# Optimization experiments

Measured on AMD Instinct MI355X. Metric: run time of the kernel, lower is better.

The kernel has to match this reference:

```python
import jax, jax.numpy as jnp
import numpy as np

BS, TGT, SRC = 16, 100, 100
M, N, H = 512, 512, 256  # query_size, key_size, hidden (min//2)


def setup_inputs() -> dict:
    key = jax.random.key(0)
    ks = jax.random.split(key, 7)
    s1 = 1.0 / np.sqrt(M + N)  # torch Linear init scale for layer 1 (fan_in = 1024)
    s2 = 1.0 / np.sqrt(H)
    return {
        "query": jax.random.normal(ks[0], (BS, TGT, M), jnp.float32),
        "keys": jax.random.normal(ks[1], (BS, SRC, N), jnp.float32),
        # W1 (H, M+N) split into key-part and query-part (concat order is (keys, query))
        "Wk": jax.random.uniform(ks[2], (N, H), jnp.float32, -s1, s1),
        "Wq": jax.random.uniform(ks[3], (M, H), jnp.float32, -s1, s1),
        "b1": jax.random.uniform(ks[4], (H,), jnp.float32, -s1, s1),
        "W2": jax.random.uniform(ks[5], (H, 1), jnp.float32, -s2, s2),
        "b2": jax.random.uniform(ks[6], (1,), jnp.float32, -s2, s2),
    }


def reference(query, keys, Wk, Wq, b1, W2, b2):
    # Equivalent to concat([keys_bcast, query_bcast], -1) @ W1 + b1:
    # apply the split weight to each side, then broadcast-add over the grid.
    hk = jnp.einsum("bsn,nh->bsh", keys, Wk)   # (bs, src, H)
    hq = jnp.einsum("btm,mh->bth", query, Wq)  # (bs, tgt, H)
    h = jnp.tanh(hk[:, :, None, :] + hq[:, None, :, :] + b1)  # (bs, src, tgt, H)
    score = jnp.tanh(jnp.einsum("bsth,ho->bsto", h, W2) + b2)  # (bs, src, tgt, 1)
    return score.squeeze(-1)  # (bs, src, tgt)
```

## Files before the change

kernel.cpp:

```cpp
#include <hip/hip_runtime.h>

#define TGT 100
#define SRC 100
#define KDIM 512
#define HH 256
#define ROWS 1600
#define LOG2E2 2.8853900817779268f

typedef __attribute__((ext_vector_type(8))) short bf16x8;
typedef __attribute__((ext_vector_type(4))) float f32x4;

static __device__ __forceinline__ unsigned short f2b(float f) {
    union { float f; unsigned u; } v; v.f = f;
    unsigned r = (v.u + 0x7FFFu + ((v.u >> 16) & 1u)) >> 16;
    return (unsigned short)r;
}

__global__ __launch_bounds__(64) void gemm_exp_kernel(
    const float* __restrict__ query,
    const float* __restrict__ keys,
    const float* __restrict__ Wk,
    const float* __restrict__ Wq,
    const float* __restrict__ b1,
    float* __restrict__ Ek, float* __restrict__ EqT)
{
    const int lane = threadIdx.x & 63;
    const int m = lane & 15, q = lane >> 4;
    const int bx = blockIdx.x;
    const int rt = bx >> 4;
    const int h0 = (bx & 15) << 4;
    const bool isq = rt >= 100;
    const float* A = isq ? query : keys;
    const float* W = isq ? Wq : Wk;
    const int r0 = (isq ? rt - 100 : rt) << 4;
    const float* arow = A + (size_t)(r0 + m) * KDIM;

    f32x4 acc = {0.f, 0.f, 0.f, 0.f};
    for (int kk = 0; kk < 16; ++kk) {
        const int kb = kk * 32 + q * 8;
        f32x4 a0 = *(const f32x4*)(arow + kb);
        f32x4 a1 = *(const f32x4*)(arow + kb + 4);
        bf16x8 afrag, bfrag;
        #pragma unroll
        for (int j = 0; j < 4; ++j) { afrag[j] = (short)f2b(a0[j]); afrag[j+4] = (short)f2b(a1[j]); }
        const float* wp = W + (size_t)kb * HH + h0 + m;
        #pragma unroll
        for (int j = 0; j < 8; ++j) bfrag[j] = (short)f2b(wp[j * HH]);
        acc = __builtin_amdgcn_mfma_f32_16x16x32_bf16(afrag, bfrag, acc, 0, 0, 0);
    }

    const int hc = h0 + m;
    if (!isq) {
        #pragma unroll
        for (int r = 0; r < 4; ++r) {
            const int row = r0 + q * 4 + r;
            Ek[(size_t)row * HH + hc] = __builtin_amdgcn_exp2f(LOG2E2 * acc[r]);
        }
    } else {
        const float bb = b1[hc];
        #pragma unroll
        for (int r = 0; r < 4; ++r) {
            const int row = r0 + q * 4 + r;
            EqT[(size_t)hc * ROWS + row] =
                __builtin_amdgcn_exp2f(LOG2E2 * (acc[r] + bb));
        }
    }
}

__global__ __launch_bounds__(64) void score_kernel(
    const float* __restrict__ Ek, const float* __restrict__ EqT,
    const float* __restrict__ W2, const float* __restrict__ B2,
    float* __restrict__ out)
{
    const int lane = threadIdx.x & 63;
    const int bx = blockIdx.x;
    const int tc = (bx & 1) << 6;
    const int g  = bx >> 1;
    const int sp = g % 50;
    const int b  = g / 50;
    const int s0 = sp * 2;
    const int t  = tc + lane;
    const int tcl = t < TGT ? t : TGT - 1;

    const float* __restrict__ ek0 = Ek + (size_t)(b * SRC + s0) * HH;
    const float* __restrict__ ek1 = ek0 + HH;
    const float* __restrict__ eq  = EqT + (size_t)b * TGT + tcl;

    float acc0 = 0.f, acc1 = 0.f;
    #pragma unroll 4
    for (int hp = 0; hp < HH / 2; ++hp) {
        const int h = hp * 2;
        const float w0 = W2[h], w1 = W2[h + 1];
        const float e0 = eq[(size_t)h * ROWS];
        const float e1 = eq[(size_t)(h + 1) * ROWS];
        const float ka0 = ek0[h], ka1 = ek0[h + 1];
        const float kb0 = ek1[h], kb1 = ek1[h + 1];
        acc0 = fmaf(w0, __builtin_amdgcn_rcpf(fmaf(ka0, e0, 1.0f)), acc0);
        acc1 = fmaf(w0, __builtin_amdgcn_rcpf(fmaf(kb0, e0, 1.0f)), acc1);
        acc0 = fmaf(w1, __builtin_amdgcn_rcpf(fmaf(ka1, e1, 1.0f)), acc0);
        acc1 = fmaf(w1, __builtin_amdgcn_rcpf(fmaf(kb1, e1, 1.0f)), acc1);
    }

    float sw = W2[lane] + W2[lane + 64] + W2[lane + 128] + W2[lane + 192];
    #pragma unroll
    for (int off = 32; off; off >>= 1) sw += __shfl_xor(sw, off, 64);
    const float bias = B2[0];

    if (t < TGT) {
        float* o = out + ((size_t)b * SRC + s0) * TGT + t;
        const float x0 = sw - 2.f * acc0 + bias;
        const float g0 = __builtin_amdgcn_exp2f(LOG2E2 * x0);
        o[0]   = 1.f - 2.f * __builtin_amdgcn_rcpf(g0 + 1.f);
        const float x1 = sw - 2.f * acc1 + bias;
        const float g1 = __builtin_amdgcn_exp2f(LOG2E2 * x1);
        o[TGT] = 1.f - 2.f * __builtin_amdgcn_rcpf(g1 + 1.f);
    }
}

extern "C" void kernel_launch(void* const* d_in, const int* in_sizes, int n_in,
                              void* d_out, int out_size, void* d_ws, size_t ws_size,
                              hipStream_t stream) {
    const float* query = (const float*)d_in[0];
    const float* keys  = (const float*)d_in[1];
    const float* Wk    = (const float*)d_in[2];
    const float* Wq    = (const float*)d_in[3];
    const float* b1    = (const float*)d_in[4];
    const float* W2    = (const float*)d_in[5];
    const float* B2    = (const float*)d_in[6];
    float* out = (float*)d_out;

    float* Ek  = (float*)d_ws;
    float* EqT = Ek + (size_t)ROWS * HH;

    gemm_exp_kernel<<<3200, 64, 0, stream>>>(query, keys, Wk, Wq, b1, Ek, EqT);
    score_kernel<<<1600, 64, 0, stream>>>(Ek, EqT, W2, B2, out);
}
```

Before: 105.2 us.

## Pre-pack bf16 MFMA fragments and split score reduction across four waves

A new prep kernel converts query, keys and both weight matrices to bf16 and stores them in MFMA fragment order, so the GEMM kernel does only contiguous vector loads and no per-block conversions or strided weight reads. The GEMM and score kernels now use 256-thread blocks of four waves. In the score kernel each wave handles a quarter of the hidden dimension, and the partial sums are combined through shared memory. The cost is an extra kernel launch, workspace traffic for the packed copies, and a block-level sync in the score kernel.

```diff
diff --git a/kernel.cpp b/kernel.cpp
--- a/kernel.cpp
+++ b/kernel.cpp
@@ -10,46 +10,77 @@
 typedef __attribute__((ext_vector_type(8))) short bf16x8;
 typedef __attribute__((ext_vector_type(4))) float f32x4;
 
-static __device__ __forceinline__ unsigned short f2b(float f) {
+#define EQT_OFF 409600
+#define PK_FLOAT_OFF 819200
+#define APK_SHORTS 1638400
+
+static __device__ __forceinline__ short f2b(float f) {
     union { float f; unsigned u; } v; v.f = f;
-    unsigned r = (v.u + 0x7FFFu + ((v.u >> 16) & 1u)) >> 16;
-    return (unsigned short)r;
+    return (short)((v.u + 0x7FFFu + ((v.u >> 16) & 1u)) >> 16);
 }
 
-__global__ __launch_bounds__(64) void gemm_exp_kernel(
-    const float* __restrict__ query,
-    const float* __restrict__ keys,
-    const float* __restrict__ Wk,
-    const float* __restrict__ Wq,
+__global__ __launch_bounds__(256) void prep_kernel(
+    const float* __restrict__ query, const float* __restrict__ keys,
+    const float* __restrict__ Wk, const float* __restrict__ Wq,
+    short* __restrict__ Apk, short* __restrict__ Bpk)
+{
+    const int tid = blockIdx.x * 256 + threadIdx.x;
+    if (tid < 204800) {
+        const int lane = tid & 63;
+        const int rest = tid >> 6;
+        const int kk = rest & 15;
+        const int rg = rest >> 4;
+        const float* A = (rg >= 100) ? query : keys;
+        const int r = (rg % 100) * 16 + (lane & 15);
+        const int kb = kk * 32 + (lane >> 4) * 8;
+        const float* src = A + (size_t)r * KDIM + kb;
+        f32x4 a0 = *(const f32x4*)src;
+        f32x4 a1 = *(const f32x4*)(src + 4);
+        bf16x8 v;
+        #pragma unroll
+        for (int j = 0; j < 4; ++j) { v[j] = f2b(a0[j]); v[j + 4] = f2b(a1[j]); }
+        *(bf16x8*)(Apk + (size_t)tid * 8) = v;
+    } else if (tid < 237568) {
+        const int t2 = tid - 204800;
+        const int lane = t2 & 63;
+        const int rest = t2 >> 6;
+        const int kk = rest & 15;
+        const int ht = (rest >> 4) & 15;
+        const float* W = (rest >> 8) ? Wq : Wk;
+        const int kb = kk * 32 + (lane >> 4) * 8;
+        const int col = ht * 16 + (lane & 15);
+        const float* wp = W + (size_t)kb * HH + col;
+        bf16x8 v;
+        #pragma unroll
+        for (int j = 0; j < 8; ++j) v[j] = f2b(wp[(size_t)j * HH]);
+        *(bf16x8*)(Bpk + (size_t)t2 * 8) = v;
+    }
+}
+
+__global__ __launch_bounds__(256) void gemm_exp_kernel(
+    const short* __restrict__ Apk, const short* __restrict__ Bpk,
     const float* __restrict__ b1,
     float* __restrict__ Ek, float* __restrict__ EqT)
 {
     const int lane = threadIdx.x & 63;
-    const int m = lane & 15, q = lane >> 4;
-    const int bx = blockIdx.x;
-    const int rt = bx >> 4;
-    const int h0 = (bx & 15) << 4;
-    const bool isq = rt >= 100;
-    const float* A = isq ? query : keys;
-    const float* W = isq ? Wq : Wk;
-    const int r0 = (isq ? rt - 100 : rt) << 4;
-    const float* arow = A + (size_t)(r0 + m) * KDIM;
+    const int w = blockIdx.x * 4 + (threadIdx.x >> 6);
+    const int rt = w >> 4;
+    const int ht = w & 15;
+    const int isq = rt >= 100;
+    const short* ap = Apk + ((size_t)(rt * 16) * 64 + lane) * 8;
+    const short* bp = Bpk + ((size_t)((isq * 16 + ht) * 16) * 64 + lane) * 8;
 
     f32x4 acc = {0.f, 0.f, 0.f, 0.f};
+    #pragma unroll
     for (int kk = 0; kk < 16; ++kk) {
-        const int kb = kk * 32 + q * 8;
-        f32x4 a0 = *(const f32x4*)(arow + kb);
-        f32x4 a1 = *(const f32x4*)(arow + kb + 4);
-        bf16x8 afrag, bfrag;
-        #pragma unroll
-        for (int j = 0; j < 4; ++j) { afrag[j] = (short)f2b(a0[j]); afrag[j+4] = (short)f2b(a1[j]); }
-        const float* wp = W + (size_t)kb * HH + h0 + m;
-        #pragma unroll
-        for (int j = 0; j < 8; ++j) bfrag[j] = (short)f2b(wp[j * HH]);
-        acc = __builtin_amdgcn_mfma_f32_16x16x32_bf16(afrag, bfrag, acc, 0, 0, 0);
+        bf16x8 af = *(const bf16x8*)(ap + (size_t)kk * 512);
+        bf16x8 bf = *(const bf16x8*)(bp + (size_t)kk * 512);
+        acc = __builtin_amdgcn_mfma_f32_16x16x32_bf16(af, bf, acc, 0, 0, 0);
     }
 
-    const int hc = h0 + m;
+    const int m = lane & 15, q = lane >> 4;
+    const int hc = ht * 16 + m;
+    const int r0 = (isq ? rt - 100 : rt) * 16;
     if (!isq) {
         #pragma unroll
         for (int r = 0; r < 4; ++r) {
@@ -67,12 +98,14 @@
     }
 }
 
-__global__ __launch_bounds__(64) void score_kernel(
+__global__ __launch_bounds__(256) void score_kernel(
     const float* __restrict__ Ek, const float* __restrict__ EqT,
     const float* __restrict__ W2, const float* __restrict__ B2,
     float* __restrict__ out)
 {
+    __shared__ float red[2][4][64];
     const int lane = threadIdx.x & 63;
+    const int wv = threadIdx.x >> 6;
     const int bx = blockIdx.x;
     const int tc = (bx & 1) << 6;
     const int g  = bx >> 1;
@@ -81,16 +114,17 @@
     const int s0 = sp * 2;
     const int t  = tc + lane;
     const int tcl = t < TGT ? t : TGT - 1;
+    const int h0 = wv * 64;
 
-    const float* __restrict__ ek0 = Ek + (size_t)(b * SRC + s0) * HH;
+    const float* __restrict__ ek0 = Ek + (size_t)(b * SRC + s0) * HH + h0;
     const float* __restrict__ ek1 = ek0 + HH;
-    const float* __restrict__ eq  = EqT + (size_t)b * TGT + tcl;
+    const float* __restrict__ eq  = EqT + (size_t)h0 * ROWS + (size_t)b * TGT + tcl;
 
     float acc0 = 0.f, acc1 = 0.f;
     #pragma unroll 4
-    for (int hp = 0; hp < HH / 2; ++hp) {
+    for (int hp = 0; hp < 32; ++hp) {
         const int h = hp * 2;
-        const float w0 = W2[h], w1 = W2[h + 1];
+        const float w0 = W2[h0 + h], w1 = W2[h0 + h + 1];
         const float e0 = eq[(size_t)h * ROWS];
         const float e1 = eq[(size_t)(h + 1) * ROWS];
         const float ka0 = ek0[h], ka1 = ek0[h + 1];
@@ -100,20 +134,20 @@
         acc0 = fmaf(w1, __builtin_amdgcn_rcpf(fmaf(ka1, e1, 1.0f)), acc0);
         acc1 = fmaf(w1, __builtin_amdgcn_rcpf(fmaf(kb1, e1, 1.0f)), acc1);
     }
+    red[0][wv][lane] = acc0;
+    red[1][wv][lane] = acc1;
+    __syncthreads();
 
-    float sw = W2[lane] + W2[lane + 64] + W2[lane + 128] + W2[lane + 192];
-    #pragma unroll
-    for (int off = 32; off; off >>= 1) sw += __shfl_xor(sw, off, 64);
-    const float bias = B2[0];
-
-    if (t < TGT) {
-        float* o = out + ((size_t)b * SRC + s0) * TGT + t;
-        const float x0 = sw - 2.f * acc0 + bias;
-        const float g0 = __builtin_amdgcn_exp2f(LOG2E2 * x0);
-        o[0]   = 1.f - 2.f * __builtin_amdgcn_rcpf(g0 + 1.f);
-        const float x1 = sw - 2.f * acc1 + bias;
-        const float g1 = __builtin_amdgcn_exp2f(LOG2E2 * x1);
-        o[TGT] = 1.f - 2.f * __builtin_amdgcn_rcpf(g1 + 1.f);
+    if (wv < 2) {
+        float a = red[wv][0][lane] + red[wv][1][lane] + red[wv][2][lane] + red[wv][3][lane];
+        float sw = W2[lane] + W2[lane + 64] + W2[lane + 128] + W2[lane + 192];
+        #pragma unroll
+        for (int off = 32; off; off >>= 1) sw += __shfl_xor(sw, off, 64);
+        const float x = sw - 2.f * a + B2[0];
+        const float gx = __builtin_amdgcn_exp2f(LOG2E2 * x);
+        if (t < TGT)
+            out[((size_t)b * SRC + s0 + wv) * TGT + t] =
+                1.f - 2.f * __builtin_amdgcn_rcpf(gx + 1.f);
     }
 }
 
@@ -130,8 +164,11 @@
     float* out = (float*)d_out;
 
     float* Ek  = (float*)d_ws;
-    float* EqT = Ek + (size_t)ROWS * HH;
+    float* EqT = Ek + EQT_OFF;
+    short* Apk = (short*)(Ek + PK_FLOAT_OFF);
+    short* Bpk = Apk + APK_SHORTS;
 
-    gemm_exp_kernel<<<3200, 64, 0, stream>>>(query, keys, Wk, Wq, b1, Ek, EqT);
-    score_kernel<<<1600, 64, 0, stream>>>(Ek, EqT, W2, B2, out);
+    prep_kernel<<<928, 256, 0, stream>>>(query, keys, Wk, Wq, Apk, Bpk);
+    gemm_exp_kernel<<<800, 256, 0, stream>>>(Apk, Bpk, b1, Ek, EqT);
+    score_kernel<<<1600, 256, 0, stream>>>(Ek, EqT, W2, B2, out);
 }
```

Result: faster. 93.77 us (-10.8%).
